# Kernel optimization log

Measured on AMD Instinct MI355X. Metric: run time of the kernel, lower is better.

Reference implementation:

```python
import jax, jax.numpy as jnp
import numpy as np


def _dot_prod_attention(h, enc):
    # h: (B,T,H), enc: (B,S,H) used as both keys and values
    att = jnp.einsum('bth,bsh->bts', h, enc)      # (B,T,S)
    att = jax.nn.softmax(att, axis=-1)
    ctx = jnp.einsum('bts,bsh->bth', att, enc)    # (B,T,H)
    return ctx, att


def setup_inputs() -> dict:
    key = jax.random.key(0)
    ks = jax.random.split(key, 7)
    B, T, S, St, H = 8, 1024, 1024, 512, 1024
    scale = 1.0 / np.sqrt(H)
    return {
        'output': jax.random.normal(ks[0], (B, T, H), dtype=jnp.float32),
        'sent': jax.random.normal(ks[1], (B, S, H), dtype=jnp.float32),
        'template': jax.random.normal(ks[2], (B, St, H), dtype=jnp.float32),
        'W_gate': jax.random.normal(ks[3], (H, 3 * H), dtype=jnp.float32) * scale,
        'W_sent': jax.random.normal(ks[4], (H, H), dtype=jnp.float32) * scale,
        'W_template': jax.random.normal(ks[5], (H, H), dtype=jnp.float32) * scale,
        'W_output': jax.random.normal(ks[6], (H, H), dtype=jnp.float32) * scale,
    }


def reference(output, sent, template, W_gate, W_sent, W_template, W_output):
    sent_ctx, sent_weight = _dot_prod_attention(output, sent)
    template_ctx, template_weight = _dot_prod_attention(output, template)

    cat = jnp.concatenate([sent_ctx, template_ctx, output], axis=-1)  # (B,T,3H)
    gate = jax.nn.sigmoid(jnp.einsum('btk,hk->bth', cat, W_gate))     # (B,T,H)

    fusion = ((1.0 - gate) * jnp.einsum('bth,kh->btk', sent_ctx, W_sent)
              + gate * jnp.einsum('bth,kh->btk', template_ctx, W_template)
              + jnp.einsum('bth,kh->btk', output, W_output))
    fusion = jnp.tanh(fusion)
    return fusion, sent_weight, template_weight
```

## Files before the change

### kernel.cpp

```cpp
#include <hip/hip_runtime.h>
#include <stdint.h>

typedef unsigned short u16;
typedef float f32x4 __attribute__((ext_vector_type(4)));
typedef int   i32x4 __attribute__((ext_vector_type(4)));

__device__ __forceinline__ u16 f2h(float f) {
  _Float16 h = (_Float16)f;
  u16 u; __builtin_memcpy(&u, &h, 2); return u;
}
__device__ __forceinline__ float h2f(u16 u) {
  _Float16 h; __builtin_memcpy(&h, &u, 2); return (float)h;
}

__device__ __forceinline__ void mfma_f16(f32x4& c, i32x4 a, i32x4 b) {
  asm("v_mfma_f32_16x16x32_f16 %0, %1, %2, %0" : "+v"(c) : "v"(a), "v"(b));
}

__device__ __forceinline__ void g2l16(const u16* g, u16* l) {
  __builtin_amdgcn_global_load_lds((const __attribute__((address_space(1))) void*)g,
                                   (__attribute__((address_space(3))) void*)l,
                                   16, 0, 0);
}

__device__ __forceinline__ void xcd_swz(int& bx, int& by, int& bz) {
  const int gx = gridDim.x, gy = gridDim.y;
  const int n = gx * gy * gridDim.z;
  const int lin = blockIdx.x + gx * (blockIdx.y + gy * blockIdx.z);
  const int q = n >> 3;
  const int s = (lin & 7) * q + (lin >> 3);
  bx = s % gx;
  const int t = s / gx;
  by = t % gy;
  bz = t / gy;
}

struct alignas(8) US4 { u16 a, b, c, d; };

__global__ void k_conv_hilo(const float* __restrict__ src, u16* __restrict__ hi,
                            u16* __restrict__ lo, int n4) {
  int i = blockIdx.x * blockDim.x + threadIdx.x;
  int stride = gridDim.x * blockDim.x;
  for (; i < n4; i += stride) {
    float4 v = reinterpret_cast<const float4*>(src)[i];
    US4 h, l;
    h.a = f2h(v.x); l.a = f2h(v.x - h2f(h.a));
    h.b = f2h(v.y); l.b = f2h(v.y - h2f(h.b));
    h.c = f2h(v.z); l.c = f2h(v.z - h2f(h.c));
    h.d = f2h(v.w); l.d = f2h(v.w - h2f(h.d));
    reinterpret_cast<US4*>(hi)[i] = h;
    reinterpret_cast<US4*>(lo)[i] = l;
  }
}

__global__ void k_conv_w(const float* __restrict__ s_wg, const float* __restrict__ s_ws,
                         const float* __restrict__ s_wt, const float* __restrict__ s_wo,
                         u16* __restrict__ d_wg, u16* __restrict__ d_ws,
                         u16* __restrict__ d_wt, u16* __restrict__ d_wo) {
  constexpr int N1 = 786432;
  constexpr int N2 = 262144;
  constexpr int total = N1 + 3 * N2;
  int i = blockIdx.x * blockDim.x + threadIdx.x;
  int stride = gridDim.x * blockDim.x;
  for (; i < total; i += stride) {
    const float* s; u16* d; int j;
    if (i < N1)                { s = s_wg; d = d_wg; j = i; }
    else if (i < N1 + N2)      { s = s_ws; d = d_ws; j = i - N1; }
    else if (i < N1 + 2 * N2)  { s = s_wt; d = d_wt; j = i - N1 - N2; }
    else                       { s = s_wo; d = d_wo; j = i - N1 - 2 * N2; }
    float4 v = reinterpret_cast<const float4*>(s)[j];
    US4 h; h.a = f2h(v.x); h.b = f2h(v.y); h.c = f2h(v.z); h.d = f2h(v.w);
    reinterpret_cast<US4*>(d)[j] = h;
  }
}

__global__ __launch_bounds__(256)
void k_conv_T(const float* __restrict__ src, u16* __restrict__ dh, u16* __restrict__ dl,
              u16* __restrict__ dt, int R, int C) {
  __shared__ u16 t[32][33];
  const int b = blockIdx.z;
  const float* s = src + (size_t)b * R * C;
  u16* dhb = dh + (size_t)b * R * C;
  u16* dlb = dl + (size_t)b * R * C;
  u16* dtb = dt + (size_t)b * R * C;
  const int c0 = blockIdx.x * 32, r0 = blockIdx.y * 32;
  const int tx = threadIdx.x, ty = threadIdx.y;
#pragma unroll
  for (int j = ty; j < 32; j += 8) {
    const size_t idx = (size_t)(r0 + j) * C + (c0 + tx);
    float x = s[idx];
    u16 h = f2h(x);
    dhb[idx] = h;
    dlb[idx] = f2h(x - h2f(h));
    t[j][tx] = h;
  }
  __syncthreads();
#pragma unroll
  for (int j = ty; j < 32; j += 8)
    dtb[(size_t)(c0 + j) * R + (r0 + tx)] = t[tx][j];
}

template<int L>
__global__ __launch_bounds__(256)
void k_softmax(float* __restrict__ io, u16* __restrict__ pb) {
  const int lane = threadIdx.x & 63;
  const size_t r = (size_t)blockIdx.x * 4 + (threadIdx.x >> 6);
  float* row = io + r * L;
  u16* prow = pb + r * L;
  constexpr int NV = L / 64;
  float v[NV];
  float mx = -3.4e38f;
#pragma unroll
  for (int j = 0; j < NV; ++j) { v[j] = row[lane + j * 64]; mx = fmaxf(mx, v[j]); }
#pragma unroll
  for (int s = 32; s; s >>= 1) mx = fmaxf(mx, __shfl_xor(mx, s));
  float sum = 0.f;
#pragma unroll
  for (int j = 0; j < NV; ++j) { v[j] = __expf(v[j] - mx); sum += v[j]; }
#pragma unroll
  for (int s = 32; s; s >>= 1) sum += __shfl_xor(sum, s);
  const float inv = 1.f / sum;
#pragma unroll
  for (int j = 0; j < NV; ++j) {
    float pv = v[j] * inv;
    row[lane + j * 64] = pv;
    prow[lane + j * 64] = f2h(pv);
  }
}

constexpr int BM = 128, BN = 128, BK = 32;

struct TC { int wv, sr, sc, wm, wn, fr, kq; };

__device__ __forceinline__ TC make_tc(int tid) {
  TC t;
  const int lane = tid & 63;
  t.wv = tid >> 6;
  t.sr = lane >> 2;
  t.sc = (lane & 3) * 8;
  t.wm = t.wv >> 1;
  t.wn = t.wv & 1;
  t.fr = lane & 15;
  t.kq = (lane >> 4) * 8;
  return t;
}

template<int SPLIT>
__device__ __forceinline__ void gemm_pass(
    f32x4 (&acc)[16],
    const u16* __restrict__ A, const u16* __restrict__ Al, int lda,
    const u16* __restrict__ B, const u16* __restrict__ Bl, int ldb,
    int K, u16* sA, u16* sAl, u16* sB, u16* sBl, const TC& t)
{
  const int nt = K / BK;
  auto stage = [&](int c, int k0) {
    u16* dA = sA + c * (BM * BK);
    u16* dB = sB + c * (BN * BK);
    const u16* ar = A + (size_t)t.sr * lda + k0 + t.sc;
    const u16* br = B + (size_t)t.sr * ldb + k0 + t.sc;
    g2l16(ar + (size_t)(t.wv * 16) * lda, dA + (t.wv * 16) * BK);
    g2l16(ar + (size_t)((t.wv + 4) * 16) * lda, dA + ((t.wv + 4) * 16) * BK);
    g2l16(br + (size_t)(t.wv * 16) * ldb, dB + (t.wv * 16) * BK);
    g2l16(br + (size_t)((t.wv + 4) * 16) * ldb, dB + ((t.wv + 4) * 16) * BK);
    if constexpr (SPLIT) {
      u16* dAl = sAl + c * (BM * BK);
      u16* dBl = sBl + c * (BN * BK);
      const u16* alr = Al + (size_t)t.sr * lda + k0 + t.sc;
      const u16* blr = Bl + (size_t)t.sr * ldb + k0 + t.sc;
      g2l16(alr + (size_t)(t.wv * 16) * lda, dAl + (t.wv * 16) * BK);
      g2l16(alr + (size_t)((t.wv + 4) * 16) * lda, dAl + ((t.wv + 4) * 16) * BK);
      g2l16(blr + (size_t)(t.wv * 16) * ldb, dBl + (t.wv * 16) * BK);
      g2l16(blr + (size_t)((t.wv + 4) * 16) * ldb, dBl + ((t.wv + 4) * 16) * BK);
    }
  };

  stage(0, 0);
  __syncthreads();
  int c = 0;
  for (int it = 0; it < nt; ++it) {
    if (it + 1 < nt) stage(c ^ 1, (it + 1) * BK);
    const u16* bA = sA + c * (BM * BK);
    const u16* bB = sB + c * (BN * BK);
    i32x4 ah[4], bh[4];
#pragma unroll
    for (int i = 0; i < 4; ++i) {
      ah[i] = *reinterpret_cast<const i32x4*>(&bA[(t.wm * 64 + i * 16 + t.fr) * BK + t.kq]);
      bh[i] = *reinterpret_cast<const i32x4*>(&bB[(t.wn * 64 + i * 16 + t.fr) * BK + t.kq]);
    }
    if constexpr (SPLIT) {
      const u16* bAl = sAl + c * (BM * BK);
      const u16* bBl = sBl + c * (BN * BK);
      i32x4 al[4], bl[4];
#pragma unroll
      for (int i = 0; i < 4; ++i) {
        al[i] = *reinterpret_cast<const i32x4*>(&bAl[(t.wm * 64 + i * 16 + t.fr) * BK + t.kq]);
        bl[i] = *reinterpret_cast<const i32x4*>(&bBl[(t.wn * 64 + i * 16 + t.fr) * BK + t.kq]);
      }
#pragma unroll
      for (int i = 0; i < 4; ++i)
#pragma unroll
        for (int j = 0; j < 4; ++j) {
          mfma_f16(acc[i * 4 + j], ah[i], bh[j]);
          mfma_f16(acc[i * 4 + j], al[i], bh[j]);
          mfma_f16(acc[i * 4 + j], ah[i], bl[j]);
        }
    } else {
#pragma unroll
      for (int i = 0; i < 4; ++i)
#pragma unroll
        for (int j = 0; j < 4; ++j)
          mfma_f16(acc[i * 4 + j], ah[i], bh[j]);
    }
    __syncthreads();
    c ^= 1;
  }
}

template<int SPLIT, int EPI>
__global__ __launch_bounds__(256, 2)
void k_gemm_nt(const u16* __restrict__ A0, const u16* __restrict__ A1, const u16* __restrict__ A2,
               const u16* __restrict__ Alo,
               const u16* __restrict__ Bm, const u16* __restrict__ Blo,
               int lda, int ldb, long long strA, long long strB,
               float* __restrict__ Cf, u16* __restrict__ Cb, int ldc, long long strC,
               int segK, int nseg)
{
  __shared__ __align__(16) u16 sA[2 * BM * BK];
  __shared__ __align__(16) u16 sB[2 * BN * BK];
  __shared__ __align__(16) u16 sAl[SPLIT ? 2 * BM * BK : 8];
  __shared__ __align__(16) u16 sBl[SPLIT ? 2 * BN * BK : 8];

  int bx, by, bz;
  xcd_swz(bx, by, bz);
  const TC t = make_tc(threadIdx.x);

  const size_t aoff = (size_t)((long long)bz * strA) + (size_t)by * BM * lda;
  const size_t boff = (size_t)((long long)bz * strB) + (size_t)bx * BN * ldb;

  f32x4 acc[16];
#pragma unroll
  for (int i = 0; i < 16; ++i) acc[i] = f32x4{0.f, 0.f, 0.f, 0.f};

  const u16* As[3] = {A0, A1, A2};
  for (int s = 0; s < nseg; ++s) {
    gemm_pass<SPLIT>(acc, As[s] + aoff, SPLIT ? Alo + aoff : nullptr, lda,
                     Bm + boff + (size_t)s * segK, SPLIT ? Blo + boff : nullptr, ldb,
                     segK, sA, sAl, sB, sBl, t);
  }

  const size_t cbse = (size_t)((long long)bz * strC);
  const int row0 = by * BM + t.wm * 64;
  const int col0 = bx * BN + t.wn * 64;
  const int fq = ((threadIdx.x & 63) >> 4) * 4;
#pragma unroll
  for (int i = 0; i < 4; ++i) {
#pragma unroll
    for (int j = 0; j < 4; ++j) {
      f32x4 v = acc[i * 4 + j];
      const int c = col0 + j * 16 + t.fr;
#pragma unroll
      for (int q = 0; q < 4; ++q) {
        const int r = row0 + i * 16 + fq + q;
        const size_t idx = cbse + (size_t)r * ldc + c;
        if constexpr (EPI == 0) {
          Cf[idx] = v[q];
        } else if constexpr (EPI == 2) {
          Cb[idx] = f2h(v[q]);
        } else {
          Cb[idx] = f2h(1.f / (1.f + __expf(-v[q])));
        }
      }
    }
  }
}

__global__ __launch_bounds__(256, 2)
void k_fusion(const u16* __restrict__ ctx_s, const u16* __restrict__ ctx_t,
              const u16* __restrict__ outh,
              const u16* __restrict__ Ws, const u16* __restrict__ Wt,
              const u16* __restrict__ Wo,
              const u16* __restrict__ g16, float* __restrict__ fus)
{
  constexpr int H = 1024;
  __shared__ __align__(16) u16 sA[2 * BM * BK];
  __shared__ __align__(16) u16 sB[2 * BN * BK];

  int bx, by, bz;
  xcd_swz(bx, by, bz);
  const TC t = make_tc(threadIdx.x);

  const size_t aoff = (size_t)by * BM * H;
  const size_t boff = (size_t)bx * BN * H;

  const int row0 = by * BM + t.wm * 64;
  const int col0 = bx * BN + t.wn * 64;
  const int fq = ((threadIdx.x & 63) >> 4) * 4;

  f32x4 acc[16];
#pragma unroll
  for (int i = 0; i < 16; ++i) acc[i] = f32x4{0.f, 0.f, 0.f, 0.f};

  gemm_pass<0>(acc, ctx_s + aoff, nullptr, H, Ws + boff, nullptr, H, H,
               sA, nullptr, sB, nullptr, t);
  f32x4 S[16];
#pragma unroll
  for (int i = 0; i < 16; ++i) { S[i] = acc[i]; acc[i] = f32x4{0.f, 0.f, 0.f, 0.f}; }

  gemm_pass<0>(acc, ctx_t + aoff, nullptr, H, Wt + boff, nullptr, H, H,
               sA, nullptr, sB, nullptr, t);
#pragma unroll
  for (int i = 0; i < 4; ++i) {
#pragma unroll
    for (int j = 0; j < 4; ++j) {
      const int c = col0 + j * 16 + t.fr;
#pragma unroll
      for (int q = 0; q < 4; ++q) {
        const int r = row0 + i * 16 + fq + q;
        const float gv = h2f(g16[(size_t)r * H + c]);
        const float sv = S[i * 4 + j][q];
        S[i * 4 + j][q] = sv + gv * (acc[i * 4 + j][q] - sv);
      }
    }
  }
#pragma unroll
  for (int i = 0; i < 16; ++i) acc[i] = f32x4{0.f, 0.f, 0.f, 0.f};

  gemm_pass<0>(acc, outh + aoff, nullptr, H, Wo + boff, nullptr, H, H,
               sA, nullptr, sB, nullptr, t);
#pragma unroll
  for (int i = 0; i < 4; ++i) {
#pragma unroll
    for (int j = 0; j < 4; ++j) {
      const int c = col0 + j * 16 + t.fr;
#pragma unroll
      for (int q = 0; q < 4; ++q) {
        const int r = row0 + i * 16 + fq + q;
        float x = S[i * 4 + j][q] + acc[i * 4 + j][q];
        float ax = fabsf(x);
        float e = __expf(-2.f * ax);
        float th = (1.f - e) / (1.f + e);
        fus[(size_t)r * H + c] = copysignf(th, x);
      }
    }
  }
}

extern "C" void kernel_launch(void* const* d_in, const int* in_sizes, int n_in,
                              void* d_out, int out_size, void* d_ws, size_t ws_size,
                              hipStream_t stream) {
  (void)in_sizes; (void)n_in; (void)out_size; (void)ws_size;
  constexpr int B = 8, T = 1024, S = 1024, St = 512, H = 1024;
  constexpr long long BTH = (long long)B * T * H;
  constexpr long long BSH = (long long)B * S * H;
  constexpr long long BStH = (long long)B * St * H;
  constexpr long long BTS = (long long)B * T * S;
  constexpr long long BTSt = (long long)B * T * St;
  constexpr long long TH = (long long)T * H;

  const float* in_out  = (const float*)d_in[0];
  const float* in_sent = (const float*)d_in[1];
  const float* in_tmpl = (const float*)d_in[2];
  const float* in_Wg   = (const float*)d_in[3];
  const float* in_Ws   = (const float*)d_in[4];
  const float* in_Wt   = (const float*)d_in[5];
  const float* in_Wo   = (const float*)d_in[6];

  float* fus = (float*)d_out;
  float* sw  = fus + BTH;
  float* tw  = sw + BTS;

  char* p = (char*)d_ws;
  auto take = [&](long long bytes) { char* q = p; p += bytes; return q; };
  u16* out_h   = (u16*)take(BTH * 2);
  u16* out_lo  = (u16*)take(BTH * 2);
  u16* sent_h  = (u16*)take(BSH * 2);
  u16* sent_lo = (u16*)take(BSH * 2);
  u16* tmpl_h  = (u16*)take(BStH * 2);
  u16* tmpl_lo = (u16*)take(BStH * 2);
  u16* sentT   = (u16*)take(BSH * 2);
  u16* tmplT   = (u16*)take(BStH * 2);
  u16* Wg_h    = (u16*)take((long long)3 * H * H * 2);
  u16* Ws_h    = (u16*)take((long long)H * H * 2);
  u16* Wt_h    = (u16*)take((long long)H * H * 2);
  u16* Wo_h    = (u16*)take((long long)H * H * 2);
  u16* Ps      = (u16*)take(BTS * 2);
  u16* Pt      = (u16*)take(BTSt * 2);
  u16* g16     = (u16*)take(BTH * 2);

  u16* ctx_s = sent_h;
  u16* ctx_t = sent_lo;

  dim3 thr(256);

  k_conv_hilo<<<2048, 256, 0, stream>>>(in_out, out_h, out_lo, (int)(BTH / 4));
  k_conv_w<<<1024, 256, 0, stream>>>(in_Wg, in_Ws, in_Wt, in_Wo, Wg_h, Ws_h, Wt_h, Wo_h);
  k_conv_T<<<dim3(H / 32, S / 32, B), dim3(32, 8), 0, stream>>>(in_sent, sent_h, sent_lo, sentT, S, H);
  k_conv_T<<<dim3(H / 32, St / 32, B), dim3(32, 8), 0, stream>>>(in_tmpl, tmpl_h, tmpl_lo, tmplT, St, H);

  k_gemm_nt<1, 0><<<dim3(S / BN, T / BM, B), thr, 0, stream>>>(
      out_h, nullptr, nullptr, out_lo, sent_h, sent_lo, H, H, TH, (long long)S * H,
      sw, nullptr, S, (long long)T * S, H, 1);
  k_gemm_nt<1, 0><<<dim3(St / BN, T / BM, B), thr, 0, stream>>>(
      out_h, nullptr, nullptr, out_lo, tmpl_h, tmpl_lo, H, H, TH, (long long)St * H,
      tw, nullptr, St, (long long)T * St, H, 1);

  k_softmax<1024><<<(B * T) / 4, 256, 0, stream>>>(sw, Ps);
  k_softmax<512><<<(B * T) / 4, 256, 0, stream>>>(tw, Pt);

  k_gemm_nt<0, 2><<<dim3(H / BN, T / BM, B), thr, 0, stream>>>(
      Ps, nullptr, nullptr, nullptr, sentT, nullptr, S, S, (long long)T * S, (long long)H * S,
      nullptr, ctx_s, H, TH, S, 1);
  k_gemm_nt<0, 2><<<dim3(H / BN, T / BM, B), thr, 0, stream>>>(
      Pt, nullptr, nullptr, nullptr, tmplT, nullptr, St, St, (long long)T * St, (long long)H * St,
      nullptr, ctx_t, H, TH, St, 1);

  k_gemm_nt<0, 6><<<dim3(H / BN, (B * T) / BM, 1), thr, 0, stream>>>(
      ctx_s, ctx_t, out_h, nullptr, Wg_h, nullptr, H, 3 * H, 0LL, 0LL,
      nullptr, g16, H, 0LL, H, 3);

  k_fusion<<<dim3(H / BN, (B * T) / BM, 1), thr, 0, stream>>>(
      ctx_s, ctx_t, out_h, Ws_h, Wt_h, Wo_h, g16, fus);
}
```

Measured before the change: 407.8 us.

## Shrink GEMM tile N to 64, raise occupancy, use MFMA builtin

```diff
diff --git a/kernel.cpp b/kernel.cpp
--- a/kernel.cpp
+++ b/kernel.cpp
@@ -2,8 +2,8 @@
 #include <stdint.h>
 
 typedef unsigned short u16;
-typedef float f32x4 __attribute__((ext_vector_type(4)));
-typedef int   i32x4 __attribute__((ext_vector_type(4)));
+typedef float    f32x4 __attribute__((ext_vector_type(4)));
+typedef _Float16 f16x8 __attribute__((ext_vector_type(8)));
 
 __device__ __forceinline__ u16 f2h(float f) {
   _Float16 h = (_Float16)f;
@@ -13,8 +13,8 @@
   _Float16 h; __builtin_memcpy(&h, &u, 2); return (float)h;
 }
 
-__device__ __forceinline__ void mfma_f16(f32x4& c, i32x4 a, i32x4 b) {
-  asm("v_mfma_f32_16x16x32_f16 %0, %1, %2, %0" : "+v"(c) : "v"(a), "v"(b));
+__device__ __forceinline__ void mfma_f16(f32x4& c, f16x8 a, f16x8 b) {
+  c = __builtin_amdgcn_mfma_f32_16x16x32_f16(a, b, c, 0, 0, 0);
 }
 
 __device__ __forceinline__ void g2l16(const u16* g, u16* l) {
@@ -128,7 +128,7 @@
   }
 }
 
-constexpr int BM = 128, BN = 128, BK = 32;
+constexpr int BM = 128, BN = 64, BK = 32;
 
 struct TC { int wv, sr, sc, wm, wn, fr, kq; };
 
@@ -147,7 +147,7 @@
 
 template<int SPLIT>
 __device__ __forceinline__ void gemm_pass(
-    f32x4 (&acc)[16],
+    f32x4 (&acc)[8],
     const u16* __restrict__ A, const u16* __restrict__ Al, int lda,
     const u16* __restrict__ B, const u16* __restrict__ Bl, int ldb,
     int K, u16* sA, u16* sAl, u16* sB, u16* sBl, const TC& t)
@@ -161,7 +161,6 @@
     g2l16(ar + (size_t)(t.wv * 16) * lda, dA + (t.wv * 16) * BK);
     g2l16(ar + (size_t)((t.wv + 4) * 16) * lda, dA + ((t.wv + 4) * 16) * BK);
     g2l16(br + (size_t)(t.wv * 16) * ldb, dB + (t.wv * 16) * BK);
-    g2l16(br + (size_t)((t.wv + 4) * 16) * ldb, dB + ((t.wv + 4) * 16) * BK);
     if constexpr (SPLIT) {
       u16* dAl = sAl + c * (BM * BK);
       u16* dBl = sBl + c * (BN * BK);
@@ -170,7 +169,6 @@
       g2l16(alr + (size_t)(t.wv * 16) * lda, dAl + (t.wv * 16) * BK);
       g2l16(alr + (size_t)((t.wv + 4) * 16) * lda, dAl + ((t.wv + 4) * 16) * BK);
       g2l16(blr + (size_t)(t.wv * 16) * ldb, dBl + (t.wv * 16) * BK);
-      g2l16(blr + (size_t)((t.wv + 4) * 16) * ldb, dBl + ((t.wv + 4) * 16) * BK);
     }
   };
 
@@ -181,35 +179,37 @@
     if (it + 1 < nt) stage(c ^ 1, (it + 1) * BK);
     const u16* bA = sA + c * (BM * BK);
     const u16* bB = sB + c * (BN * BK);
-    i32x4 ah[4], bh[4];
-#pragma unroll
-    for (int i = 0; i < 4; ++i) {
-      ah[i] = *reinterpret_cast<const i32x4*>(&bA[(t.wm * 64 + i * 16 + t.fr) * BK + t.kq]);
-      bh[i] = *reinterpret_cast<const i32x4*>(&bB[(t.wn * 64 + i * 16 + t.fr) * BK + t.kq]);
-    }
+    f16x8 ah[4], bh[2];
+#pragma unroll
+    for (int i = 0; i < 4; ++i)
+      ah[i] = *reinterpret_cast<const f16x8*>(&bA[(t.wm * 64 + i * 16 + t.fr) * BK + t.kq]);
+#pragma unroll
+    for (int j = 0; j < 2; ++j)
+      bh[j] = *reinterpret_cast<const f16x8*>(&bB[(t.wn * 32 + j * 16 + t.fr) * BK + t.kq]);
     if constexpr (SPLIT) {
       const u16* bAl = sAl + c * (BM * BK);
       const u16* bBl = sBl + c * (BN * BK);
-      i32x4 al[4], bl[4];
-#pragma unroll
-      for (int i = 0; i < 4; ++i) {
-        al[i] = *reinterpret_cast<const i32x4*>(&bAl[(t.wm * 64 + i * 16 + t.fr) * BK + t.kq]);
-        bl[i] = *reinterpret_cast<const i32x4*>(&bBl[(t.wn * 64 + i * 16 + t.fr) * BK + t.kq]);
-      }
+      f16x8 al[4], bl[2];
 #pragma unroll
       for (int i = 0; i < 4; ++i)
-#pragma unroll
-        for (int j = 0; j < 4; ++j) {
-          mfma_f16(acc[i * 4 + j], ah[i], bh[j]);
-          mfma_f16(acc[i * 4 + j], al[i], bh[j]);
-          mfma_f16(acc[i * 4 + j], ah[i], bl[j]);
+        al[i] = *reinterpret_cast<const f16x8*>(&bAl[(t.wm * 64 + i * 16 + t.fr) * BK + t.kq]);
+#pragma unroll
+      for (int j = 0; j < 2; ++j)
+        bl[j] = *reinterpret_cast<const f16x8*>(&bBl[(t.wn * 32 + j * 16 + t.fr) * BK + t.kq]);
+#pragma unroll
+      for (int i = 0; i < 4; ++i)
+#pragma unroll
+        for (int j = 0; j < 2; ++j) {
+          mfma_f16(acc[i * 2 + j], ah[i], bh[j]);
+          mfma_f16(acc[i * 2 + j], al[i], bh[j]);
+          mfma_f16(acc[i * 2 + j], ah[i], bl[j]);
         }
     } else {
 #pragma unroll
       for (int i = 0; i < 4; ++i)
 #pragma unroll
-        for (int j = 0; j < 4; ++j)
-          mfma_f16(acc[i * 4 + j], ah[i], bh[j]);
+        for (int j = 0; j < 2; ++j)
+          mfma_f16(acc[i * 2 + j], ah[i], bh[j]);
     }
     __syncthreads();
     c ^= 1;
@@ -217,7 +217,7 @@
 }
 
 template<int SPLIT, int EPI>
-__global__ __launch_bounds__(256, 2)
+__global__ __launch_bounds__(256, SPLIT ? 3 : 4)
 void k_gemm_nt(const u16* __restrict__ A0, const u16* __restrict__ A1, const u16* __restrict__ A2,
                const u16* __restrict__ Alo,
                const u16* __restrict__ Bm, const u16* __restrict__ Blo,
@@ -237,9 +237,9 @@
   const size_t aoff = (size_t)((long long)bz * strA) + (size_t)by * BM * lda;
   const size_t boff = (size_t)((long long)bz * strB) + (size_t)bx * BN * ldb;
 
-  f32x4 acc[16];
-#pragma unroll
-  for (int i = 0; i < 16; ++i) acc[i] = f32x4{0.f, 0.f, 0.f, 0.f};
+  f32x4 acc[8];
+#pragma unroll
+  for (int i = 0; i < 8; ++i) acc[i] = f32x4{0.f, 0.f, 0.f, 0.f};
 
   const u16* As[3] = {A0, A1, A2};
   for (int s = 0; s < nseg; ++s) {
@@ -250,13 +250,13 @@
 
   const size_t cbse = (size_t)((long long)bz * strC);
   const int row0 = by * BM + t.wm * 64;
-  const int col0 = bx * BN + t.wn * 64;
+  const int col0 = bx * BN + t.wn * 32;
   const int fq = ((threadIdx.x & 63) >> 4) * 4;
 #pragma unroll
   for (int i = 0; i < 4; ++i) {
 #pragma unroll
-    for (int j = 0; j < 4; ++j) {
-      f32x4 v = acc[i * 4 + j];
+    for (int j = 0; j < 2; ++j) {
+      f32x4 v = acc[i * 2 + j];
       const int c = col0 + j * 16 + t.fr;
 #pragma unroll
       for (int q = 0; q < 4; ++q) {
@@ -274,7 +274,7 @@
   }
 }
 
-__global__ __launch_bounds__(256, 2)
+__global__ __launch_bounds__(256, 4)
 void k_fusion(const u16* __restrict__ ctx_s, const u16* __restrict__ ctx_t,
               const u16* __restrict__ outh,
               const u16* __restrict__ Ws, const u16* __restrict__ Wt,
@@ -293,49 +293,49 @@
   const size_t boff = (size_t)bx * BN * H;
 
   const int row0 = by * BM + t.wm * 64;
-  const int col0 = bx * BN + t.wn * 64;
+  const int col0 = bx * BN + t.wn * 32;
   const int fq = ((threadIdx.x & 63) >> 4) * 4;
 
-  f32x4 acc[16];
-#pragma unroll
-  for (int i = 0; i < 16; ++i) acc[i] = f32x4{0.f, 0.f, 0.f, 0.f};
+  f32x4 acc[8];
+#pragma unroll
+  for (int i = 0; i < 8; ++i) acc[i] = f32x4{0.f, 0.f, 0.f, 0.f};
 
   gemm_pass<0>(acc, ctx_s + aoff, nullptr, H, Ws + boff, nullptr, H, H,
                sA, nullptr, sB, nullptr, t);
-  f32x4 S[16];
-#pragma unroll
-  for (int i = 0; i < 16; ++i) { S[i] = acc[i]; acc[i] = f32x4{0.f, 0.f, 0.f, 0.f}; }
+  f32x4 S[8];
+#pragma unroll
+  for (int i = 0; i < 8; ++i) { S[i] = acc[i]; acc[i] = f32x4{0.f, 0.f, 0.f, 0.f}; }
 
   gemm_pass<0>(acc, ctx_t + aoff, nullptr, H, Wt + boff, nullptr, H, H,
                sA, nullptr, sB, nullptr, t);
 #pragma unroll
   for (int i = 0; i < 4; ++i) {
 #pragma unroll
-    for (int j = 0; j < 4; ++j) {
+    for (int j = 0; j < 2; ++j) {
       const int c = col0 + j * 16 + t.fr;
 #pragma unroll
       for (int q = 0; q < 4; ++q) {
         const int r = row0 + i * 16 + fq + q;
         const float gv = h2f(g16[(size_t)r * H + c]);
-        const float sv = S[i * 4 + j][q];
-        S[i * 4 + j][q] = sv + gv * (acc[i * 4 + j][q] - sv);
+        const float sv = S[i * 2 + j][q];
+        S[i * 2 + j][q] = sv + gv * (acc[i * 2 + j][q] - sv);
       }
     }
   }
 #pragma unroll
-  for (int i = 0; i < 16; ++i) acc[i] = f32x4{0.f, 0.f, 0.f, 0.f};
+  for (int i = 0; i < 8; ++i) acc[i] = f32x4{0.f, 0.f, 0.f, 0.f};
 
   gemm_pass<0>(acc, outh + aoff, nullptr, H, Wo + boff, nullptr, H, H,
                sA, nullptr, sB, nullptr, t);
 #pragma unroll
   for (int i = 0; i < 4; ++i) {
 #pragma unroll
-    for (int j = 0; j < 4; ++j) {
+    for (int j = 0; j < 2; ++j) {
       const int c = col0 + j * 16 + t.fr;
 #pragma unroll
       for (int q = 0; q < 4; ++q) {
         const int r = row0 + i * 16 + fq + q;
-        float x = S[i * 4 + j][q] + acc[i * 4 + j][q];
+        float x = S[i * 2 + j][q] + acc[i * 2 + j][q];
         float ax = fabsf(x);
         float e = __expf(-2.f * ax);
         float th = (1.f - e) / (1.f + e);
```

Result: slower. 436.7 us (+7.1%).

## Triple-buffer GEMM LDS staging with vmcnt waits and narrower split-precision tiles

Applied to the files above, without the earlier changes.

```diff
diff --git a/kernel.cpp b/kernel.cpp
--- a/kernel.cpp
+++ b/kernel.cpp
@@ -2,8 +2,8 @@
 #include <stdint.h>
 
 typedef unsigned short u16;
-typedef float f32x4 __attribute__((ext_vector_type(4)));
-typedef int   i32x4 __attribute__((ext_vector_type(4)));
+typedef float    f32x4 __attribute__((ext_vector_type(4)));
+typedef _Float16 f16x8 __attribute__((ext_vector_type(8)));
 
 __device__ __forceinline__ u16 f2h(float f) {
   _Float16 h = (_Float16)f;
@@ -13,14 +13,26 @@
   _Float16 h; __builtin_memcpy(&h, &u, 2); return (float)h;
 }
 
-__device__ __forceinline__ void mfma_f16(f32x4& c, i32x4 a, i32x4 b) {
-  asm("v_mfma_f32_16x16x32_f16 %0, %1, %2, %0" : "+v"(c) : "v"(a), "v"(b));
+__device__ __forceinline__ void mfma_f16(f32x4& c, f16x8 a, f16x8 b) {
+  c = __builtin_amdgcn_mfma_f32_16x16x32_f16(a, b, c, 0, 0, 0);
 }
 
 __device__ __forceinline__ void g2l16(const u16* g, u16* l) {
   __builtin_amdgcn_global_load_lds((const __attribute__((address_space(1))) void*)g,
                                    (__attribute__((address_space(3))) void*)l,
                                    16, 0, 0);
+}
+
+template<int N>
+__device__ __forceinline__ void s_waitcnt_vm() {
+  if constexpr (N == 0) asm volatile("s_waitcnt vmcnt(0)" ::: "memory");
+  else if constexpr (N == 1) asm volatile("s_waitcnt vmcnt(1)" ::: "memory");
+  else if constexpr (N == 2) asm volatile("s_waitcnt vmcnt(2)" ::: "memory");
+  else if constexpr (N == 3) asm volatile("s_waitcnt vmcnt(3)" ::: "memory");
+  else if constexpr (N == 4) asm volatile("s_waitcnt vmcnt(4)" ::: "memory");
+  else if constexpr (N == 5) asm volatile("s_waitcnt vmcnt(5)" ::: "memory");
+  else if constexpr (N == 6) asm volatile("s_waitcnt vmcnt(6)" ::: "memory");
+  else if constexpr (N == 8) asm volatile("s_waitcnt vmcnt(8)" ::: "memory");
 }
 
 __device__ __forceinline__ void xcd_swz(int& bx, int& by, int& bz) {
@@ -128,7 +140,7 @@
   }
 }
 
-constexpr int BM = 128, BN = 128, BK = 32;
+constexpr int BM = 128, BK = 32;
 
 struct TC { int wv, sr, sc, wm, wn, fr, kq; };
 
@@ -145,74 +157,91 @@
   return t;
 }
 
-template<int SPLIT>
+template<int SPLIT, int BNN>
 __device__ __forceinline__ void gemm_pass(
-    f32x4 (&acc)[16],
+    f32x4* acc,
     const u16* __restrict__ A, const u16* __restrict__ Al, int lda,
     const u16* __restrict__ B, const u16* __restrict__ Bl, int ldb,
     int K, u16* sA, u16* sAl, u16* sB, u16* sBl, const TC& t)
 {
+  constexpr int NB  = BNN / 32;
+  constexpr int BCH = BNN / 64;
+  constexpr int LPS = (2 + BCH) * (SPLIT ? 2 : 1);
+  constexpr int ASZ = BM * BK, BSZ = BNN * BK;
   const int nt = K / BK;
+
   auto stage = [&](int c, int k0) {
-    u16* dA = sA + c * (BM * BK);
-    u16* dB = sB + c * (BN * BK);
+    u16* dA = sA + c * ASZ;
+    u16* dB = sB + c * BSZ;
     const u16* ar = A + (size_t)t.sr * lda + k0 + t.sc;
     const u16* br = B + (size_t)t.sr * ldb + k0 + t.sc;
     g2l16(ar + (size_t)(t.wv * 16) * lda, dA + (t.wv * 16) * BK);
     g2l16(ar + (size_t)((t.wv + 4) * 16) * lda, dA + ((t.wv + 4) * 16) * BK);
     g2l16(br + (size_t)(t.wv * 16) * ldb, dB + (t.wv * 16) * BK);
-    g2l16(br + (size_t)((t.wv + 4) * 16) * ldb, dB + ((t.wv + 4) * 16) * BK);
+    if constexpr (BCH == 2)
+      g2l16(br + (size_t)((t.wv + 4) * 16) * ldb, dB + ((t.wv + 4) * 16) * BK);
     if constexpr (SPLIT) {
-      u16* dAl = sAl + c * (BM * BK);
-      u16* dBl = sBl + c * (BN * BK);
+      u16* dAl = sAl + c * ASZ;
+      u16* dBl = sBl + c * BSZ;
       const u16* alr = Al + (size_t)t.sr * lda + k0 + t.sc;
       const u16* blr = Bl + (size_t)t.sr * ldb + k0 + t.sc;
       g2l16(alr + (size_t)(t.wv * 16) * lda, dAl + (t.wv * 16) * BK);
       g2l16(alr + (size_t)((t.wv + 4) * 16) * lda, dAl + ((t.wv + 4) * 16) * BK);
       g2l16(blr + (size_t)(t.wv * 16) * ldb, dBl + (t.wv * 16) * BK);
-      g2l16(blr + (size_t)((t.wv + 4) * 16) * ldb, dBl + ((t.wv + 4) * 16) * BK);
+      if constexpr (BCH == 2)
+        g2l16(blr + (size_t)((t.wv + 4) * 16) * ldb, dBl + ((t.wv + 4) * 16) * BK);
     }
   };
 
   stage(0, 0);
-  __syncthreads();
-  int c = 0;
+  stage(1, BK);
+  s_waitcnt_vm<LPS>();
+  __builtin_amdgcn_s_barrier();
+  __builtin_amdgcn_sched_barrier(0);
+
   for (int it = 0; it < nt; ++it) {
-    if (it + 1 < nt) stage(c ^ 1, (it + 1) * BK);
-    const u16* bA = sA + c * (BM * BK);
-    const u16* bB = sB + c * (BN * BK);
-    i32x4 ah[4], bh[4];
-#pragma unroll
-    for (int i = 0; i < 4; ++i) {
-      ah[i] = *reinterpret_cast<const i32x4*>(&bA[(t.wm * 64 + i * 16 + t.fr) * BK + t.kq]);
-      bh[i] = *reinterpret_cast<const i32x4*>(&bB[(t.wn * 64 + i * 16 + t.fr) * BK + t.kq]);
-    }
+    const int cb = it % 3;
+    if (it + 2 < nt) stage((it + 2) % 3, (it + 2) * BK);
+
+    const u16* bA = sA + cb * ASZ;
+    const u16* bB = sB + cb * BSZ;
+    f16x8 ah[4], bh[NB];
+#pragma unroll
+    for (int i = 0; i < 4; ++i)
+      ah[i] = *reinterpret_cast<const f16x8*>(&bA[(t.wm * 64 + i * 16 + t.fr) * BK + t.kq]);
+#pragma unroll
+    for (int j = 0; j < NB; ++j)
+      bh[j] = *reinterpret_cast<const f16x8*>(&bB[(t.wn * (BNN / 2) + j * 16 + t.fr) * BK + t.kq]);
     if constexpr (SPLIT) {
-      const u16* bAl = sAl + c * (BM * BK);
-      const u16* bBl = sBl + c * (BN * BK);
-      i32x4 al[4], bl[4];
-#pragma unroll
-      for (int i = 0; i < 4; ++i) {
-        al[i] = *reinterpret_cast<const i32x4*>(&bAl[(t.wm * 64 + i * 16 + t.fr) * BK + t.kq]);
-        bl[i] = *reinterpret_cast<const i32x4*>(&bBl[(t.wn * 64 + i * 16 + t.fr) * BK + t.kq]);
-      }
+      const u16* bAl = sAl + cb * ASZ;
+      const u16* bBl = sBl + cb * BSZ;
+      f16x8 al[4], bl[NB];
 #pragma unroll
       for (int i = 0; i < 4; ++i)
-#pragma unroll
-        for (int j = 0; j < 4; ++j) {
-          mfma_f16(acc[i * 4 + j], ah[i], bh[j]);
-          mfma_f16(acc[i * 4 + j], al[i], bh[j]);
-          mfma_f16(acc[i * 4 + j], ah[i], bl[j]);
+        al[i] = *reinterpret_cast<const f16x8*>(&bAl[(t.wm * 64 + i * 16 + t.fr) * BK + t.kq]);
+#pragma unroll
+      for (int j = 0; j < NB; ++j)
+        bl[j] = *reinterpret_cast<const f16x8*>(&bBl[(t.wn * (BNN / 2) + j * 16 + t.fr) * BK + t.kq]);
+#pragma unroll
+      for (int i = 0; i < 4; ++i)
+#pragma unroll
+        for (int j = 0; j < NB; ++j) {
+          mfma_f16(acc[i * NB + j], ah[i], bh[j]);
+          mfma_f16(acc[i * NB + j], al[i], bh[j]);
+          mfma_f16(acc[i * NB + j], ah[i], bl[j]);
         }
     } else {
 #pragma unroll
       for (int i = 0; i < 4; ++i)
 #pragma unroll
-        for (int j = 0; j < 4; ++j)
-          mfma_f16(acc[i * 4 + j], ah[i], bh[j]);
+        for (int j = 0; j < NB; ++j)
+          mfma_f16(acc[i * NB + j], ah[i], bh[j]);
     }
-    __syncthreads();
-    c ^= 1;
+
+    if (it + 2 < nt)      s_waitcnt_vm<LPS>();
+    else if (it + 1 < nt) s_waitcnt_vm<0>();
+    __builtin_amdgcn_s_barrier();
+    __builtin_amdgcn_sched_barrier(0);
   }
 }
 
@@ -225,38 +254,40 @@
                float* __restrict__ Cf, u16* __restrict__ Cb, int ldc, long long strC,
                int segK, int nseg)
 {
-  __shared__ __align__(16) u16 sA[2 * BM * BK];
-  __shared__ __align__(16) u16 sB[2 * BN * BK];
-  __shared__ __align__(16) u16 sAl[SPLIT ? 2 * BM * BK : 8];
-  __shared__ __align__(16) u16 sBl[SPLIT ? 2 * BN * BK : 8];
+  constexpr int BNN = SPLIT ? 64 : 128;
+  constexpr int NB = BNN / 32;
+  __shared__ __align__(16) u16 sA[3 * BM * BK];
+  __shared__ __align__(16) u16 sB[3 * BNN * BK];
+  __shared__ __align__(16) u16 sAl[SPLIT ? 3 * BM * BK : 8];
+  __shared__ __align__(16) u16 sBl[SPLIT ? 3 * BNN * BK : 8];
 
   int bx, by, bz;
   xcd_swz(bx, by, bz);
   const TC t = make_tc(threadIdx.x);
 
   const size_t aoff = (size_t)((long long)bz * strA) + (size_t)by * BM * lda;
-  const size_t boff = (size_t)((long long)bz * strB) + (size_t)bx * BN * ldb;
-
-  f32x4 acc[16];
-#pragma unroll
-  for (int i = 0; i < 16; ++i) acc[i] = f32x4{0.f, 0.f, 0.f, 0.f};
+  const size_t boff = (size_t)((long long)bz * strB) + (size_t)bx * BNN * ldb;
+
+  f32x4 acc[4 * NB];
+#pragma unroll
+  for (int i = 0; i < 4 * NB; ++i) acc[i] = f32x4{0.f, 0.f, 0.f, 0.f};
 
   const u16* As[3] = {A0, A1, A2};
   for (int s = 0; s < nseg; ++s) {
-    gemm_pass<SPLIT>(acc, As[s] + aoff, SPLIT ? Alo + aoff : nullptr, lda,
-                     Bm + boff + (size_t)s * segK, SPLIT ? Blo + boff : nullptr, ldb,
-                     segK, sA, sAl, sB, sBl, t);
+    gemm_pass<SPLIT, BNN>(acc, As[s] + aoff, SPLIT ? Alo + aoff : nullptr, lda,
+                          Bm + boff + (size_t)s * segK, SPLIT ? Blo + boff : nullptr, ldb,
+                          segK, sA, sAl, sB, sBl, t);
   }
 
   const size_t cbse = (size_t)((long long)bz * strC);
   const int row0 = by * BM + t.wm * 64;
-  const int col0 = bx * BN + t.wn * 64;
+  const int col0 = bx * BNN + t.wn * (BNN / 2);
   const int fq = ((threadIdx.x & 63) >> 4) * 4;
 #pragma unroll
   for (int i = 0; i < 4; ++i) {
 #pragma unroll
-    for (int j = 0; j < 4; ++j) {
-      f32x4 v = acc[i * 4 + j];
+    for (int j = 0; j < NB; ++j) {
+      f32x4 v = acc[i * NB + j];
       const int c = col0 + j * 16 + t.fr;
 #pragma unroll
       for (int q = 0; q < 4; ++q) {
@@ -282,32 +313,32 @@
               const u16* __restrict__ g16, float* __restrict__ fus)
 {
   constexpr int H = 1024;
-  __shared__ __align__(16) u16 sA[2 * BM * BK];
-  __shared__ __align__(16) u16 sB[2 * BN * BK];
+  __shared__ __align__(16) u16 sA[3 * BM * BK];
+  __shared__ __align__(16) u16 sB[3 * 128 * BK];
 
   int bx, by, bz;
   xcd_swz(bx, by, bz);
   const TC t = make_tc(threadIdx.x);
 
   const size_t aoff = (size_t)by * BM * H;
-  const size_t boff = (size_t)bx * BN * H;
+  const size_t boff = (size_t)bx * 128 * H;
 
   const int row0 = by * BM + t.wm * 64;
-  const int col0 = bx * BN + t.wn * 64;
+  const int col0 = bx * 128 + t.wn * 64;
   const int fq = ((threadIdx.x & 63) >> 4) * 4;
 
   f32x4 acc[16];
 #pragma unroll
   for (int i = 0; i < 16; ++i) acc[i] = f32x4{0.f, 0.f, 0.f, 0.f};
 
-  gemm_pass<0>(acc, ctx_s + aoff, nullptr, H, Ws + boff, nullptr, H, H,
-               sA, nullptr, sB, nullptr, t);
+  gemm_pass<0, 128>(acc, ctx_s + aoff, nullptr, H, Ws + boff, nullptr, H, H,
+                    sA, nullptr, sB, nullptr, t);
   f32x4 S[16];
 #pragma unroll
   for (int i = 0; i < 16; ++i) { S[i] = acc[i]; acc[i] = f32x4{0.f, 0.f, 0.f, 0.f}; }
 
-  gemm_pass<0>(acc, ctx_t + aoff, nullptr, H, Wt + boff, nullptr, H, H,
-               sA, nullptr, sB, nullptr, t);
+  gemm_pass<0, 128>(acc, ctx_t + aoff, nullptr, H, Wt + boff, nullptr, H, H,
+                    sA, nullptr, sB, nullptr, t);
 #pragma unroll
   for (int i = 0; i < 4; ++i) {
 #pragma unroll
@@ -325,8 +356,8 @@
 #pragma unroll
   for (int i = 0; i < 16; ++i) acc[i] = f32x4{0.f, 0.f, 0.f, 0.f};
 
-  gemm_pass<0>(acc, outh + aoff, nullptr, H, Wo + boff, nullptr, H, H,
-               sA, nullptr, sB, nullptr, t);
+  gemm_pass<0, 128>(acc, outh + aoff, nullptr, H, Wo + boff, nullptr, H, H,
+                    sA, nullptr, sB, nullptr, t);
 #pragma unroll
   for (int i = 0; i < 4; ++i) {
 #pragma unroll
@@ -397,27 +428,27 @@
   k_conv_T<<<dim3(H / 32, S / 32, B), dim3(32, 8), 0, stream>>>(in_sent, sent_h, sent_lo, sentT, S, H);
   k_conv_T<<<dim3(H / 32, St / 32, B), dim3(32, 8), 0, stream>>>(in_tmpl, tmpl_h, tmpl_lo, tmplT, St, H);
 
-  k_gemm_nt<1, 0><<<dim3(S / BN, T / BM, B), thr, 0, stream>>>(
+  k_gemm_nt<1, 0><<<dim3(S / 64, T / BM, B), thr, 0, stream>>>(
       out_h, nullptr, nullptr, out_lo, sent_h, sent_lo, H, H, TH, (long long)S * H,
       sw, nullptr, S, (long long)T * S, H, 1);
-  k_gemm_nt<1, 0><<<dim3(St / BN, T / BM, B), thr, 0, stream>>>(
+  k_gemm_nt<1, 0><<<dim3(St / 64, T / BM, B), thr, 0, stream>>>(
       out_h, nullptr, nullptr, out_lo, tmpl_h, tmpl_lo, H, H, TH, (long long)St * H,
       tw, nullptr, St, (long long)T * St, H, 1);
 
   k_softmax<1024><<<(B * T) / 4, 256, 0, stream>>>(sw, Ps);
   k_softmax<512><<<(B * T) / 4, 256, 0, stream>>>(tw, Pt);
 
-  k_gemm_nt<0, 2><<<dim3(H / BN, T / BM, B), thr, 0, stream>>>(
+  k_gemm_nt<0, 2><<<dim3(H / 128, T / BM, B), thr, 0, stream>>>(
       Ps, nullptr, nullptr, nullptr, sentT, nullptr, S, S, (long long)T * S, (long long)H * S,
       nullptr, ctx_s, H, TH, S, 1);
-  k_gemm_nt<0, 2><<<dim3(H / BN, T / BM, B), thr, 0, stream>>>(
+  k_gemm_nt<0, 2><<<dim3(H / 128, T / BM, B), thr, 0, stream>>>(
       Pt, nullptr, nullptr, nullptr, tmplT, nullptr, St, St, (long long)T * St, (long long)H * St,
       nullptr, ctx_t, H, TH, St, 1);
 
-  k_gemm_nt<0, 6><<<dim3(H / BN, (B * T) / BM, 1), thr, 0, stream>>>(
+  k_gemm_nt<0, 6><<<dim3(H / 128, (B * T) / BM, 1), thr, 0, stream>>>(
       ctx_s, ctx_t, out_h, nullptr, Wg_h, nullptr, H, 3 * H, 0LL, 0LL,
       nullptr, g16, H, 0LL, H, 3);
 
-  k_fusion<<<dim3(H / BN, (B * T) / BM, 1), thr, 0, stream>>>(
+  k_fusion<<<dim3(H / 128, (B * T) / BM, 1), thr, 0, stream>>>(
       ctx_s, ctx_t, out_h, Ws_h, Wt_h, Wo_h, g16, fus);
 }
```

Result: slower. 423.7 us (+3.9%).
